# Kernel optimization log

Measured on AMD Instinct MI355X. Metric: run time of the kernel, lower is better.

Reference implementation:

```python
import jax, jax.numpy as jnp
import numpy as np

N = 50000
E = 1600000
D_IN = 512
EPS = 1e-5


def setup_inputs() -> dict:
    key = jax.random.key(0)
    ks = jax.random.split(key, 20)
    p = lambda k, shape: jax.random.normal(k, shape, dtype=jnp.float32) * 0.05
    return {
        "x": jax.random.normal(ks[0], (N, D_IN), dtype=jnp.float32),
        "edge_index": jax.random.randint(ks[1], (2, E), 0, N),
        "edge_weight": jax.random.uniform(ks[2], (E,), dtype=jnp.float32),
        # conv1: ChebConv(512->400) with K=1,2,3 (weight per Chebyshev order)
        "W1a": p(ks[3], (1, D_IN, 400)), "b1a": p(ks[4], (400,)),
        "W1b": p(ks[5], (2, D_IN, 400)), "b1b": p(ks[6], (400,)),
        "W1c": p(ks[7], (3, D_IN, 400)), "b1c": p(ks[8], (400,)),
        "g1": jnp.ones((1200,), jnp.float32), "beta1": jnp.zeros((1200,), jnp.float32),
        # conv2: ChebConv(1200->100) with K=1,2,3
        "W2a": p(ks[9], (1, 1200, 100)), "b2a": p(ks[10], (100,)),
        "W2b": p(ks[11], (2, 1200, 100)), "b2b": p(ks[12], (100,)),
        "W2c": p(ks[13], (3, 1200, 100)), "b2c": p(ks[14], (100,)),
        "g2": jnp.ones((300,), jnp.float32), "beta2": jnp.zeros((300,), jnp.float32),
        "Wl": p(ks[15], (300, 10)), "bl": p(ks[16], (10,)),
    }


def _cheb(x, row, col, norm, W, b):
    """PyG ChebConv forward: out = sum_k T_k(L_hat) x @ W[k] + b.
    L_hat (sym norm, lambda_max=2) = -D^{-1/2} A D^{-1/2}, zero diagonal,
    applied as scatter: (L_hat h)[col] += norm_e * h[row]."""
    K = W.shape[0]
    n = x.shape[0]
    prop = lambda h: jax.ops.segment_sum(norm[:, None] * h[row], col, num_segments=n)
    out = x @ W[0]
    Tx_prev, Tx = x, None
    if K >= 2:
        Tx = prop(x)
        out = out + Tx @ W[1]
    for k in range(2, K):
        Tx_new = 2.0 * prop(Tx) - Tx_prev
        out = out + Tx_new @ W[k]
        Tx_prev, Tx = Tx, Tx_new
    return out + b


def _bn(h, g, beta):
    # BatchNorm over nodes (training-mode batch statistics, biased var)
    mu = h.mean(axis=0)
    var = h.var(axis=0)
    return (h - mu) * jax.lax.rsqrt(var + EPS) * g + beta


def reference(x, edge_index, edge_weight, W1a, b1a, W1b, b1b, W1c, b1c, g1, beta1,
              W2a, b2a, W2b, b2b, W2c, b2c, g2, beta2, Wl, bl):
    row, col = edge_index[0], edge_index[1]
    deg = jax.ops.segment_sum(edge_weight, row, num_segments=x.shape[0])
    safe = jnp.where(deg > 0, deg, 1.0)
    dis = jnp.where(deg > 0, jax.lax.rsqrt(safe), 0.0)  # deg^{-1/2}, inf -> 0
    norm = -dis[row] * edge_weight * dis[col]  # scaled-Laplacian edge weights

    h = jnp.concatenate([
        _cheb(x, row, col, norm, W1a, b1a),
        _cheb(x, row, col, norm, W1b, b1b),
        _cheb(x, row, col, norm, W1c, b1c)], axis=1)  # [N, 1200]
    h = jax.nn.relu(_bn(h, g1, beta1))

    h = jnp.concatenate([
        _cheb(h, row, col, norm, W2a, b2a),
        _cheb(h, row, col, norm, W2b, b2b),
        _cheb(h, row, col, norm, W2c, b2c)], axis=1)  # [N, 300]
    h = _bn(h, g2, beta2)

    logits = h @ Wl + bl  # [N, 10]
    return jax.nn.log_softmax(logits, axis=1)
```

## Files before the change

kernel.cpp:

```cpp
#include <hip/hip_runtime.h>
#include <math.h>

#define EPSB 1e-5f

typedef __attribute__((ext_vector_type(8))) short short8;
typedef __attribute__((ext_vector_type(4))) float floatx4;

__device__ inline float bf2f(unsigned short h) {
  union { unsigned int u; float f; } v; v.u = ((unsigned int)h) << 16; return v.f;
}
__device__ inline unsigned short f2bf(float f) {
  union { float f; unsigned int u; } v; v.f = f;
  unsigned int r = v.u + 0x7fffu + ((v.u >> 16) & 1u);
  return (unsigned short)(r >> 16);
}

__device__ __forceinline__ void gl2lds16(const unsigned short* g, unsigned short* l) {
  __builtin_amdgcn_global_load_lds(
      (const __attribute__((address_space(1))) unsigned int*)g,
      (__attribute__((address_space(3))) unsigned int*)l, 16, 0, 0);
}


__global__ void deg_kernel(const int* __restrict__ row, const float* __restrict__ ew,
                           float* __restrict__ deg, int E) {
  int e = blockIdx.x * blockDim.x + threadIdx.x;
  if (e < E) atomicAdd(&deg[row[e]], ew[e]);
}

__global__ void dis_kernel(float* deg, int n) {
  int i = blockIdx.x * blockDim.x + threadIdx.x;
  if (i < n) { float d = deg[i]; deg[i] = d > 0.f ? rsqrtf(d) : 0.f; }
}

__global__ void count_kernel(const int* __restrict__ col, int* __restrict__ cnt, int E) {
  int e = blockIdx.x * blockDim.x + threadIdx.x;
  if (e < E) atomicAdd(&cnt[col[e]], 1);
}

__global__ __launch_bounds__(1024) void scan_kernel(const int* __restrict__ cnt,
                                                    int* __restrict__ off, int n) {
  __shared__ int buf[1024];
  __shared__ int carry;
  int tid = threadIdx.x;
  if (tid == 0) carry = 0;
  __syncthreads();
  for (int base = 0; base < n; base += 1024) {
    int idx = base + tid;
    int v = (idx < n) ? cnt[idx] : 0;
    buf[tid] = v;
    __syncthreads();
    for (int s = 1; s < 1024; s <<= 1) {
      int t = (tid >= s) ? buf[tid - s] : 0;
      __syncthreads();
      if (tid >= s) buf[tid] += t;
      __syncthreads();
    }
    int total = buf[1023];
    if (idx < n) off[idx] = carry + buf[tid] - v;
    __syncthreads();
    if (tid == 0) carry += total;
    __syncthreads();
  }
  if (tid == 0) off[n] = carry;
}

__global__ void copy_kernel(const int* __restrict__ src, int* __restrict__ dst, int n) {
  int i = blockIdx.x * blockDim.x + threadIdx.x;
  if (i < n) dst[i] = src[i];
}

__global__ void fill_kernel(const int* __restrict__ row, const int* __restrict__ col,
                            const float* __restrict__ ew, const float* __restrict__ dis,
                            int* __restrict__ wptr,
                            int2* __restrict__ ePack, int E) {
  int e = blockIdx.x * blockDim.x + threadIdx.x;
  if (e < E) {
    int r = row[e], c = col[e];
    int p = atomicAdd(&wptr[c], 1);
    float nv = -dis[r] * ew[e] * dis[c];
    ePack[p] = make_int2(r, __float_as_int(nv));
  }
}


__global__ void cast_x_kernel(const float* __restrict__ x, unsigned short* __restrict__ xb,
                              int N) {
  int idx = blockIdx.x * blockDim.x + threadIdx.x;
  if (idx >= N * 128) return;
  int row = idx >> 7, c4 = idx & 127;
  float4 v = *reinterpret_cast<const float4*>(x + (size_t)row * 512 + c4 * 4);
  union { unsigned int u[2]; } p;
  p.u[0] = (unsigned int)f2bf(v.x) | ((unsigned int)f2bf(v.y) << 16);
  p.u[1] = (unsigned int)f2bf(v.z) | ((unsigned int)f2bf(v.w) << 16);
  *reinterpret_cast<uint2*>(xb + (size_t)row * 1536 + c4 * 4) = make_uint2(p.u[0], p.u[1]);
}

__global__ void wprep_kernel(const float* __restrict__ W, unsigned short* __restrict__ Bt,
                             int Ktot, int Nout, int ldBt, int rowOff) {
  int idx = blockIdx.x * blockDim.x + threadIdx.x;
  if (idx >= Ktot * Nout) return;
  int k = idx / Nout, n = idx - k * Nout;
  Bt[(size_t)(rowOff + n) * ldBt + k] = f2bf(W[idx]);
}

__global__ void padzero_kernel(unsigned short* __restrict__ h, int N) {
  int i = blockIdx.x * blockDim.x + threadIdx.x;
  if (i >= N * 2) return;
  *reinterpret_cast<uint4*>(h + (size_t)(i >> 1) * 1216 + 1200 + (i & 1) * 8) =
      make_uint4(0, 0, 0, 0);
}

__global__ void bcat_kernel(const float* __restrict__ a, const float* __restrict__ b,
                            const float* __restrict__ c, float* __restrict__ dst) {
  int i = threadIdx.x;
  if (i < 100) dst[i] = a[i];
  else if (i < 200) dst[i] = b[i - 100];
  else if (i < 300) dst[i] = c[i - 200];
}

__device__ inline void acc8(float* a, uint4 g, float w) {
  a[0] += w * bf2f((unsigned short)(g.x & 0xffff));
  a[1] += w * bf2f((unsigned short)(g.x >> 16));
  a[2] += w * bf2f((unsigned short)(g.y & 0xffff));
  a[3] += w * bf2f((unsigned short)(g.y >> 16));
  a[4] += w * bf2f((unsigned short)(g.z & 0xffff));
  a[5] += w * bf2f((unsigned short)(g.z >> 16));
  a[6] += w * bf2f((unsigned short)(g.w & 0xffff));
  a[7] += w * bf2f((unsigned short)(g.w >> 16));
}

__global__ __launch_bounds__(256) void prop_chunk_kernel(
    unsigned short* __restrict__ base, int ld,
    int srcCol, int dstCol, int subCol,
    const int* __restrict__ off, const int2* __restrict__ ePack,
    float scale, int N) {
  int chunk = blockIdx.x & 7;
  int g = blockIdx.x >> 3;
  int tid = threadIdx.x;
  int slot = (tid >> 3) & 3;
  int c8 = tid & 7;
  int v = g * 8 + (tid >> 5);
  bool valid = v < N;
  int vv = valid ? v : N - 1;
  int co = chunk * 64 + c8 * 8;
  const unsigned short* src = base + srcCol + co;
  int s = off[vv], e = off[vv + 1];
  float a[8] = {}, b[8] = {};
  int i = s + slot;
  for (; i + 12 < e; i += 16) {
    int2 p0 = ePack[i];
    int2 p1 = ePack[i + 4];
    int2 p2 = ePack[i + 8];
    int2 p3 = ePack[i + 12];
    uint4 g0 = *reinterpret_cast<const uint4*>(src + (size_t)p0.x * ld);
    uint4 g1 = *reinterpret_cast<const uint4*>(src + (size_t)p1.x * ld);
    uint4 g2 = *reinterpret_cast<const uint4*>(src + (size_t)p2.x * ld);
    uint4 g3 = *reinterpret_cast<const uint4*>(src + (size_t)p3.x * ld);
    acc8(a, g0, __int_as_float(p0.y));
    acc8(b, g1, __int_as_float(p1.y));
    acc8(a, g2, __int_as_float(p2.y));
    acc8(b, g3, __int_as_float(p3.y));
  }
  for (; i < e; i += 4) {
    int2 p = ePack[i];
    uint4 gg = *reinterpret_cast<const uint4*>(src + (size_t)p.x * ld);
    acc8(a, gg, __int_as_float(p.y));
  }
#pragma unroll
  for (int j = 0; j < 8; j++) a[j] += b[j];
#pragma unroll
  for (int j = 0; j < 8; j++) {
    a[j] += __shfl_xor(a[j], 8);
    a[j] += __shfl_xor(a[j], 16);
  }
  if (slot != 0 || !valid) return;
  if (subCol >= 0) {
    uint4 sv = *reinterpret_cast<const uint4*>(base + subCol + co + (size_t)v * ld);
    a[0] = scale * a[0] - bf2f((unsigned short)(sv.x & 0xffff));
    a[1] = scale * a[1] - bf2f((unsigned short)(sv.x >> 16));
    a[2] = scale * a[2] - bf2f((unsigned short)(sv.y & 0xffff));
    a[3] = scale * a[3] - bf2f((unsigned short)(sv.y >> 16));
    a[4] = scale * a[4] - bf2f((unsigned short)(sv.z & 0xffff));
    a[5] = scale * a[5] - bf2f((unsigned short)(sv.z >> 16));
    a[6] = scale * a[6] - bf2f((unsigned short)(sv.w & 0xffff));
    a[7] = scale * a[7] - bf2f((unsigned short)(sv.w >> 16));
  }
  uint4 o;
  o.x = (unsigned int)f2bf(a[0]) | ((unsigned int)f2bf(a[1]) << 16);
  o.y = (unsigned int)f2bf(a[2]) | ((unsigned int)f2bf(a[3]) << 16);
  o.z = (unsigned int)f2bf(a[4]) | ((unsigned int)f2bf(a[5]) << 16);
  o.w = (unsigned int)f2bf(a[6]) | ((unsigned int)f2bf(a[7]) << 16);
  *reinterpret_cast<uint4*>(base + dstCol + co + (size_t)v * ld) = o;
}

__global__ void prop_z_kernel(const unsigned short* __restrict__ Zcat,
                              const int* __restrict__ off, const int2* __restrict__ ePack,
                              float* __restrict__ h2f, unsigned short* __restrict__ U1) {
  int v = blockIdx.x;
  int f8 = threadIdx.x;
  if (f8 >= 38) return;
  int s = off[v], e = off[v + 1];
  float a[8] = {}, b[8] = {};
  int i = s;
  for (; i + 3 < e; i += 4) {
    int2 p0 = ePack[i];
    int2 p1 = ePack[i + 1];
    int2 p2 = ePack[i + 2];
    int2 p3 = ePack[i + 3];
    uint4 g0 = *reinterpret_cast<const uint4*>(Zcat + (size_t)p0.x * 304 + f8 * 8);
    uint4 g1 = *reinterpret_cast<const uint4*>(Zcat + (size_t)p1.x * 304 + f8 * 8);
    uint4 g2 = *reinterpret_cast<const uint4*>(Zcat + (size_t)p2.x * 304 + f8 * 8);
    uint4 g3 = *reinterpret_cast<const uint4*>(Zcat + (size_t)p3.x * 304 + f8 * 8);
    acc8(a, g0, __int_as_float(p0.y));
    acc8(b, g1, __int_as_float(p1.y));
    acc8(a, g2, __int_as_float(p2.y));
    acc8(b, g3, __int_as_float(p3.y));
  }
  for (; i < e; i++) {
    int2 p = ePack[i];
    uint4 raw = *reinterpret_cast<const uint4*>(Zcat + (size_t)p.x * 304 + f8 * 8);
    acc8(a, raw, __int_as_float(p.y));
  }
#pragma unroll
  for (int j = 0; j < 8; j++) a[j] += b[j];
  if (f8 < 25) {
    float* p = h2f + (size_t)v * 300 + 100 + f8 * 8;
#pragma unroll
    for (int j = 0; j < 8; j++) p[j] += a[j];
  } else {
    uint4 o;
    o.x = (unsigned int)f2bf(a[0]) | ((unsigned int)f2bf(a[1]) << 16);
    o.y = (unsigned int)f2bf(a[2]) | ((unsigned int)f2bf(a[3]) << 16);
    o.z = (unsigned int)f2bf(a[4]) | ((unsigned int)f2bf(a[5]) << 16);
    o.w = (unsigned int)f2bf(a[6]) | ((unsigned int)f2bf(a[7]) << 16);
    *reinterpret_cast<uint4*>(U1 + (size_t)v * 104 + (f8 - 25) * 8) = o;
  }
}

__global__ void prop_u_kernel(const unsigned short* __restrict__ U1,
                              const int* __restrict__ off, const int2* __restrict__ ePack,
                              const unsigned short* __restrict__ Zcat,
                              float* __restrict__ h2f) {
  int v = blockIdx.x;
  int f8 = threadIdx.x;
  if (f8 >= 13) return;
  int s = off[v], e = off[v + 1];
  float a[8] = {}, b[8] = {};
  int i = s;
  for (; i + 3 < e; i += 4) {
    int2 p0 = ePack[i];
    int2 p1 = ePack[i + 1];
    int2 p2 = ePack[i + 2];
    int2 p3 = ePack[i + 3];
    uint4 g0 = *reinterpret_cast<const uint4*>(U1 + (size_t)p0.x * 104 + f8 * 8);
    uint4 g1 = *reinterpret_cast<const uint4*>(U1 + (size_t)p1.x * 104 + f8 * 8);
    uint4 g2 = *reinterpret_cast<const uint4*>(U1 + (size_t)p2.x * 104 + f8 * 8);
    uint4 g3 = *reinterpret_cast<const uint4*>(U1 + (size_t)p3.x * 104 + f8 * 8);
    acc8(a, g0, __int_as_float(p0.y));
    acc8(b, g1, __int_as_float(p1.y));
    acc8(a, g2, __int_as_float(p2.y));
    acc8(b, g3, __int_as_float(p3.y));
  }
  for (; i < e; i++) {
    int2 p = ePack[i];
    uint4 raw = *reinterpret_cast<const uint4*>(U1 + (size_t)p.x * 104 + f8 * 8);
    acc8(a, raw, __int_as_float(p.y));
  }
#pragma unroll
  for (int j = 0; j < 8; j++) a[j] += b[j];
  const unsigned short* z2 = Zcat + (size_t)v * 304 + 200;
  float* p = h2f + (size_t)v * 300 + 200;
#pragma unroll
  for (int j = 0; j < 8; j++) {
    int c = f8 * 8 + j;
    if (c < 100) p[c] += 2.f * a[j] - bf2f(z2[c]);
  }
}

__global__ __launch_bounds__(256) void gemm_bf16_kernel(
    const unsigned short* __restrict__ A, int lda,
    const unsigned short* __restrict__ Bt, int ldb,
    int M, int Nc, int K,
    const float* __restrict__ bias,
    unsigned short* __restrict__ Cb, float* __restrict__ Cf, int ldc, int c0,
    int accumulate) {
  __shared__ __align__(16) unsigned short As[128 * 32];
  __shared__ __align__(16) unsigned short Bs[128 * 32];
  int tid = threadIdx.x;
  int wave = tid >> 6, lane = tid & 63;
  int q = lane >> 4, mn = lane & 15;
  int wr = wave >> 1, wc = wave & 1;
  int row0 = blockIdx.y * 128, col0 = blockIdx.x * 128;
  floatx4 acc[4][4] = {};

  const unsigned short* ga[2];
  const unsigned short* gb[2];
  unsigned short* la[2];
  unsigned short* lb[2];
#pragma unroll
  for (int j = 0; j < 2; j++) {
    int c = j * 256 + tid;
    int r = c >> 2, cw = (c & 3) * 8;
    int gr = row0 + r; if (gr > M - 1) gr = M - 1;
    ga[j] = A + (size_t)gr * lda + cw;
    int gn = col0 + r; if (gn > Nc - 1) gn = Nc - 1;
    gb[j] = Bt + (size_t)gn * ldb + cw;
    la[j] = &As[(j * 256 + wave * 64) * 8];
    lb[j] = &Bs[(j * 256 + wave * 64) * 8];
  }

  for (int k0 = 0; k0 < K; k0 += 32) {
#pragma unroll
    for (int j = 0; j < 2; j++) {
      gl2lds16(ga[j] + k0, la[j]);
      gl2lds16(gb[j] + k0, lb[j]);
    }
    __syncthreads();

    short8 af[4], bf[4];
#pragma unroll
    for (int i = 0; i < 4; i++) {
      af[i] = *reinterpret_cast<const short8*>(&As[(wr * 64 + i * 16 + mn) * 32 + q * 8]);
      bf[i] = *reinterpret_cast<const short8*>(&Bs[(wc * 64 + i * 16 + mn) * 32 + q * 8]);
    }
#pragma unroll
    for (int mi = 0; mi < 4; mi++)
#pragma unroll
      for (int ni = 0; ni < 4; ni++)
        acc[mi][ni] = __builtin_amdgcn_mfma_f32_16x16x32_bf16(af[mi], bf[ni], acc[mi][ni], 0, 0, 0);
    __syncthreads();
  }

#pragma unroll
  for (int mi = 0; mi < 4; mi++) {
#pragma unroll
    for (int ni = 0; ni < 4; ni++) {
      int gcol = col0 + wc * 64 + ni * 16 + mn;
      if (gcol >= Nc) continue;
      float b = bias ? bias[gcol] : 0.f;
#pragma unroll
      for (int r = 0; r < 4; r++) {
        int grow = row0 + wr * 64 + mi * 16 + q * 4 + r;
        if (grow >= M) continue;
        float v = acc[mi][ni][r] + b;
        if (Cb) {
          Cb[(size_t)grow * ldc + c0 + gcol] = f2bf(v);
        } else {
          float* p = Cf + (size_t)grow * ldc + c0 + gcol;
          if (accumulate) v += *p;
          *p = v;
        }
      }
    }
  }
}

__global__ void bn_stats_bf16_kernel(const unsigned short* __restrict__ h, int ld, int C,
                                     int N, float* __restrict__ sums) {
  int c = blockIdx.x * blockDim.x + threadIdx.x;
  if (c >= C) return;
  int r0 = blockIdx.y * 256;
  int r1 = min(N, r0 + 256);
  float s = 0.f, s2 = 0.f;
  for (int r = r0; r < r1; r++) {
    float v = bf2f(h[(size_t)r * ld + c]);
    s += v; s2 += v * v;
  }
  atomicAdd(&sums[c], s);
  atomicAdd(&sums[C + c], s2);
}

__global__ void scsh_kernel(const float* __restrict__ sums, const float* __restrict__ g,
                            const float* __restrict__ beta, float invN, int C,
                            float* __restrict__ scSh) {
  int c = blockIdx.x * blockDim.x + threadIdx.x;
  if (c >= C) return;
  float mu = sums[c] * invN;
  float var = sums[C + c] * invN - mu * mu;
  float s = rsqrtf(var + EPSB) * g[c];
  scSh[c] = s;
  scSh[C + c] = beta[c] - mu * s;
}

__global__ void bn_apply_bf16_kernel(unsigned short* __restrict__ h, int ld, int C8, int N,
                                     const float* __restrict__ scSh, int Cfull, int relu) {
  int idx = blockIdx.x * blockDim.x + threadIdx.x;
  if (idx >= N * C8) return;
  int row = idx / C8, c8 = idx - row * C8;
  unsigned short* p = h + (size_t)row * ld + c8 * 8;
  uint4 raw = *reinterpret_cast<uint4*>(p);
  float v[8];
  v[0] = bf2f((unsigned short)(raw.x & 0xffff)); v[1] = bf2f((unsigned short)(raw.x >> 16));
  v[2] = bf2f((unsigned short)(raw.y & 0xffff)); v[3] = bf2f((unsigned short)(raw.y >> 16));
  v[4] = bf2f((unsigned short)(raw.z & 0xffff)); v[5] = bf2f((unsigned short)(raw.z >> 16));
  v[6] = bf2f((unsigned short)(raw.w & 0xffff)); v[7] = bf2f((unsigned short)(raw.w >> 16));
#pragma unroll
  for (int j = 0; j < 8; j++) {
    int c = c8 * 8 + j;
    float o = v[j] * scSh[c] + scSh[Cfull + c];
    if (relu) o = fmaxf(o, 0.f);
    v[j] = o;
  }
  uint4 o;
  o.x = (unsigned int)f2bf(v[0]) | ((unsigned int)f2bf(v[1]) << 16);
  o.y = (unsigned int)f2bf(v[2]) | ((unsigned int)f2bf(v[3]) << 16);
  o.z = (unsigned int)f2bf(v[4]) | ((unsigned int)f2bf(v[5]) << 16);
  o.w = (unsigned int)f2bf(v[6]) | ((unsigned int)f2bf(v[7]) << 16);
  *reinterpret_cast<uint4*>(p) = o;
}

__global__ void bn_stats_kernel(const float* __restrict__ h, int C, int N,
                                float* __restrict__ sums) {
  int c = blockIdx.x * blockDim.x + threadIdx.x;
  if (c >= C) return;
  int r0 = blockIdx.y * 256;
  int r1 = min(N, r0 + 256);
  float s = 0.f, s2 = 0.f;
  for (int r = r0; r < r1; r++) {
    float v = h[(size_t)r * C + c];
    s += v; s2 += v * v;
  }
  atomicAdd(&sums[c], s);
  atomicAdd(&sums[C + c], s2);
}

__global__ void bn_apply_kernel(float* __restrict__ h, int C, int N,
                                const float* __restrict__ sums, const float* __restrict__ g,
                                const float* __restrict__ beta, float invN, int relu) {
  int C4 = C >> 2;
  int c4 = blockIdx.x * blockDim.x + threadIdx.x;
  if (c4 >= C4) return;
  float sc[4], sh[4];
#pragma unroll
  for (int j = 0; j < 4; j++) {
    int c = c4 * 4 + j;
    float mu = sums[c] * invN;
    float var = sums[C + c] * invN - mu * mu;
    float s = rsqrtf(var + EPSB) * g[c];
    sc[j] = s; sh[j] = beta[c] - mu * s;
  }
  int r0 = blockIdx.y * 256, r1 = min(N, r0 + 256);
  for (int r = r0; r < r1; r++) {
    float4* p = reinterpret_cast<float4*>(h + (size_t)r * C) + c4;
    float4 v = *p;
    v.x = v.x * sc[0] + sh[0]; v.y = v.y * sc[1] + sh[1];
    v.z = v.z * sc[2] + sh[2]; v.w = v.w * sc[3] + sh[3];
    if (relu) {
      v.x = fmaxf(v.x, 0.f); v.y = fmaxf(v.y, 0.f);
      v.z = fmaxf(v.z, 0.f); v.w = fmaxf(v.w, 0.f);
    }
    *p = v;
  }
}


__global__ __launch_bounds__(256) void final_bn_kernel(const float* __restrict__ h2,
                                                       const float* __restrict__ scSh,
                                                       const float* __restrict__ Wl,
                                                       const float* __restrict__ bl,
                                                       float* __restrict__ out, int N) {
  __shared__ float Ws[3000];
  __shared__ float S[600];
  for (int i = threadIdx.x; i < 3000; i += 256) Ws[i] = Wl[i];
  for (int i = threadIdx.x; i < 600; i += 256) S[i] = scSh[i];
  __syncthreads();
  int r = blockIdx.x * blockDim.x + threadIdx.x;
  if (r >= N) return;
  float acc[10];
#pragma unroll
  for (int c = 0; c < 10; c++) acc[c] = bl[c];
  const float* hr = h2 + (size_t)r * 300;
  for (int k = 0; k < 300; k++) {
    float x = hr[k] * S[k] + S[300 + k];
#pragma unroll
    for (int c = 0; c < 10; c++) acc[c] += x * Ws[k * 10 + c];
  }
  float mx = acc[0];
#pragma unroll
  for (int c = 1; c < 10; c++) mx = fmaxf(mx, acc[c]);
  float se = 0.f;
#pragma unroll
  for (int c = 0; c < 10; c++) se += expf(acc[c] - mx);
  float lz = mx + logf(se);
#pragma unroll
  for (int c = 0; c < 10; c++) out[(size_t)r * 10 + c] = acc[c] - lz;
}

__global__ __launch_bounds__(256) void final_kernel(const float* __restrict__ h2,
                                                    const float* __restrict__ Wl,
                                                    const float* __restrict__ bl,
                                                    float* __restrict__ out, int N) {
  __shared__ float Ws[3000];
  for (int i = threadIdx.x; i < 3000; i += 256) Ws[i] = Wl[i];
  __syncthreads();
  int r = blockIdx.x * blockDim.x + threadIdx.x;
  if (r >= N) return;
  float acc[10];
#pragma unroll
  for (int c = 0; c < 10; c++) acc[c] = bl[c];
  const float* hr = h2 + (size_t)r * 300;
  for (int k = 0; k < 300; k++) {
    float x = hr[k];
#pragma unroll
    for (int c = 0; c < 10; c++) acc[c] += x * Ws[k * 10 + c];
  }
  float mx = acc[0];
#pragma unroll
  for (int c = 1; c < 10; c++) mx = fmaxf(mx, acc[c]);
  float se = 0.f;
#pragma unroll
  for (int c = 0; c < 10; c++) se += expf(acc[c] - mx);
  float lz = mx + logf(se);
#pragma unroll
  for (int c = 0; c < 10; c++) out[(size_t)r * 10 + c] = acc[c] - lz;
}


__global__ void prop_kernel(const float* __restrict__ src, int srcLd4, int D4,
                            const int* __restrict__ off, const int2* __restrict__ ePack,
                            float* __restrict__ dst, int dstLd4,
                            const float* __restrict__ sub, int subLd4, float scale) {
  int v = blockIdx.x;
  int f4 = threadIdx.x;
  if (f4 >= D4) return;
  int s = off[v], e = off[v + 1];
  float ax = 0.f, ay = 0.f, az = 0.f, aw = 0.f;
  for (int i = s; i < e; i++) {
    int2 p = ePack[i];
    float w = __int_as_float(p.y);
    const float4 hv = *reinterpret_cast<const float4*>(src + ((size_t)p.x * srcLd4 + f4) * 4);
    ax += w * hv.x; ay += w * hv.y; az += w * hv.z; aw += w * hv.w;
  }
  float4 o;
  if (sub) {
    const float4 sv = *reinterpret_cast<const float4*>(sub + ((size_t)v * subLd4 + f4) * 4);
    o.x = scale * ax - sv.x; o.y = scale * ay - sv.y;
    o.z = scale * az - sv.z; o.w = scale * aw - sv.w;
  } else {
    o.x = ax; o.y = ay; o.z = az; o.w = aw;
  }
  *reinterpret_cast<float4*>(dst + ((size_t)v * dstLd4 + f4) * 4) = o;
}

#define BM 64
#define BN 64
#define BK 16

__global__ __launch_bounds__(256) void gemm_kernel(
    const float* __restrict__ A, int lda,
    const float* __restrict__ B, int ldb,
    float* __restrict__ C, int ldc, int c0,
    int M, int Nc, int K,
    const float* __restrict__ bias, int accumulate) {
  __shared__ float As[BK][BM + 4];
  __shared__ float Bs[BK][BN + 4];
  int tid = threadIdx.x;
  int tx = tid & 15, ty = tid >> 4;
  int row0 = blockIdx.y * BM, col0 = blockIdx.x * BN;
  float acc[4][4] = {};
  int aM = tid >> 2;
  int aK = (tid & 3) << 2;
  int bK = tid >> 4;
  int bN = (tid & 15) << 2;
  for (int k0 = 0; k0 < K; k0 += BK) {
    float4 av = make_float4(0.f, 0.f, 0.f, 0.f);
    int ar = row0 + aM;
    if (ar < M && k0 + aK < K)
      av = *reinterpret_cast<const float4*>(A + (size_t)ar * lda + k0 + aK);
    As[aK + 0][aM] = av.x; As[aK + 1][aM] = av.y;
    As[aK + 2][aM] = av.z; As[aK + 3][aM] = av.w;
    float4 bv = make_float4(0.f, 0.f, 0.f, 0.f);
    int bc = col0 + bN;
    if (bc < Nc && k0 + bK < K)
      bv = *reinterpret_cast<const float4*>(B + (size_t)(k0 + bK) * ldb + bc);
    Bs[bK][bN + 0] = bv.x; Bs[bK][bN + 1] = bv.y;
    Bs[bK][bN + 2] = bv.z; Bs[bK][bN + 3] = bv.w;
    __syncthreads();
#pragma unroll
    for (int k = 0; k < BK; k++) {
      float a0 = As[k][ty * 4 + 0], a1 = As[k][ty * 4 + 1];
      float a2 = As[k][ty * 4 + 2], a3 = As[k][ty * 4 + 3];
      float b0 = Bs[k][tx * 4 + 0], b1 = Bs[k][tx * 4 + 1];
      float b2 = Bs[k][tx * 4 + 2], b3 = Bs[k][tx * 4 + 3];
      acc[0][0] += a0 * b0; acc[0][1] += a0 * b1; acc[0][2] += a0 * b2; acc[0][3] += a0 * b3;
      acc[1][0] += a1 * b0; acc[1][1] += a1 * b1; acc[1][2] += a1 * b2; acc[1][3] += a1 * b3;
      acc[2][0] += a2 * b0; acc[2][1] += a2 * b1; acc[2][2] += a2 * b2; acc[2][3] += a2 * b3;
      acc[3][0] += a3 * b0; acc[3][1] += a3 * b1; acc[3][2] += a3 * b2; acc[3][3] += a3 * b3;
    }
    __syncthreads();
  }
#pragma unroll
  for (int i = 0; i < 4; i++) {
    int r = row0 + ty * 4 + i;
    if (r >= M) continue;
#pragma unroll
    for (int j = 0; j < 4; j++) {
      int c = col0 + tx * 4 + j;
      if (c >= Nc) continue;
      float v = acc[i][j];
      if (bias) v += bias[c];
      float* p = C + (size_t)r * ldc + c0 + c;
      if (accumulate) *p += v; else *p = v;
    }
  }
}


extern "C" void kernel_launch(void* const* d_in, const int* in_sizes, int n_in,
                              void* d_out, int out_size, void* d_ws, size_t ws_size,
                              hipStream_t stream) {
  const float* x   = (const float*)d_in[0];
  const int*   ei  = (const int*)d_in[1];
  const float* ew  = (const float*)d_in[2];
  const float* W1a = (const float*)d_in[3];
  const float* b1a = (const float*)d_in[4];
  const float* W1b = (const float*)d_in[5];
  const float* b1b = (const float*)d_in[6];
  const float* W1c = (const float*)d_in[7];
  const float* b1c = (const float*)d_in[8];
  const float* g1  = (const float*)d_in[9];
  const float* be1 = (const float*)d_in[10];
  const float* W2a = (const float*)d_in[11];
  const float* b2a = (const float*)d_in[12];
  const float* W2b = (const float*)d_in[13];
  const float* b2b = (const float*)d_in[14];
  const float* W2c = (const float*)d_in[15];
  const float* b2c = (const float*)d_in[16];
  const float* g2  = (const float*)d_in[17];
  const float* be2 = (const float*)d_in[18];
  const float* Wl  = (const float*)d_in[19];
  const float* bl  = (const float*)d_in[20];
  float* out = (float*)d_out;

  const int N = in_sizes[0] / 512;
  const int E = in_sizes[1] / 2;
  const int* row = ei;
  const int* col = ei + E;
  (void)n_in; (void)out_size;

  int eb = (E + 255) / 256;
  int nb = (N + 255) / 256;

  char* ws = (char*)d_ws;
  size_t o = 0;
  int2*  ePack = (int2*)(ws + o);  o += (size_t)E * 8;
  float* dis   = (float*)(ws + o); o += (size_t)N * 4;
  int*   cnt   = (int*)(ws + o);   o += (size_t)N * 4;
  int*   off   = (int*)(ws + o);   o += (size_t)(N + 4) * 4;
  int*   wptr  = (int*)(ws + o);   o += (size_t)N * 4;
  float* sums  = (float*)(ws + o); o += 2400 * 4;
  float* scSh  = (float*)(ws + o); o += 2400 * 4;
  float* bcat  = (float*)(ws + o); o += 304 * 4;
  o = (o + 255) & ~(size_t)255;
  size_t oCommon = o;

  size_t oA = oCommon;
  unsigned short* Bt1a = (unsigned short*)(ws + oA); oA += (size_t)400 * 512 * 2;
  unsigned short* Bt1b = (unsigned short*)(ws + oA); oA += (size_t)400 * 1024 * 2;
  unsigned short* Bt1c = (unsigned short*)(ws + oA); oA += (size_t)400 * 1536 * 2;
  unsigned short* Bt2cat0 = (unsigned short*)(ws + oA); oA += (size_t)304 * 1216 * 2;
  unsigned short* Bt2z    = (unsigned short*)(ws + oA); oA += (size_t)304 * 1216 * 2;
  oA = (oA + 255) & ~(size_t)255;
  unsigned short* h1n = (unsigned short*)(ws + oA); oA += (size_t)N * 1216 * 2;
  oA = (oA + 255) & ~(size_t)255;
  float* h2f = (float*)(ws + oA); oA += (size_t)N * 300 * 4;
  oA = (oA + 255) & ~(size_t)255;
  unsigned short* Xcat = (unsigned short*)(ws + oA); oA += (size_t)N * 1536 * 2;
  unsigned short* Zcat = Xcat;
  unsigned short* U1 = Xcat + (size_t)N * 304;

  bool planA = (ws_size >= oA);

  hipMemsetAsync(dis, 0, (size_t)N * 4, stream);
  hipMemsetAsync(cnt, 0, (size_t)N * 4, stream);
  deg_kernel<<<eb, 256, 0, stream>>>(row, ew, dis, E);
  dis_kernel<<<nb, 256, 0, stream>>>(dis, N);
  count_kernel<<<eb, 256, 0, stream>>>(col, cnt, E);
  scan_kernel<<<1, 1024, 0, stream>>>(cnt, off, N);
  copy_kernel<<<nb, 256, 0, stream>>>(off, wptr, N);
  fill_kernel<<<eb, 256, 0, stream>>>(row, col, ew, dis, wptr, ePack, E);

  if (planA) {
    wprep_kernel<<<(400 * 512 + 255) / 256, 256, 0, stream>>>(W1a, Bt1a, 512, 400, 512, 0);
    wprep_kernel<<<(400 * 1024 + 255) / 256, 256, 0, stream>>>(W1b, Bt1b, 1024, 400, 1024, 0);
    wprep_kernel<<<(400 * 1536 + 255) / 256, 256, 0, stream>>>(W1c, Bt1c, 1536, 400, 1536, 0);
    hipMemsetAsync(Bt2cat0, 0, (size_t)304 * 1216 * 2, stream);
    hipMemsetAsync(Bt2z, 0, (size_t)304 * 1216 * 2, stream);
    wprep_kernel<<<(100 * 1200 + 255) / 256, 256, 0, stream>>>(W2a, Bt2cat0, 1200, 100, 1216, 0);
    wprep_kernel<<<(100 * 1200 + 255) / 256, 256, 0, stream>>>(W2b, Bt2cat0, 1200, 100, 1216, 100);
    wprep_kernel<<<(100 * 1200 + 255) / 256, 256, 0, stream>>>(W2c, Bt2cat0, 1200, 100, 1216, 200);
    wprep_kernel<<<(100 * 1200 + 255) / 256, 256, 0, stream>>>(W2b + 1200 * 100, Bt2z, 1200, 100, 1216, 0);
    wprep_kernel<<<(100 * 1200 + 255) / 256, 256, 0, stream>>>(W2c + 1200 * 100, Bt2z, 1200, 100, 1216, 100);
    wprep_kernel<<<(100 * 1200 + 255) / 256, 256, 0, stream>>>(W2c + 2 * 1200 * 100, Bt2z, 1200, 100, 1216, 200);
    bcat_kernel<<<1, 320, 0, stream>>>(b2a, b2b, b2c, bcat);
    cast_x_kernel<<<(N * 128 + 255) / 256, 256, 0, stream>>>(x, Xcat, N);
    padzero_kernel<<<(N * 2 + 255) / 256, 256, 0, stream>>>(h1n, N);

    int gridP = ((N + 7) / 8) * 8;
    prop_chunk_kernel<<<gridP, 256, 0, stream>>>(Xcat, 1536, 0, 512, -1,
                                                 off, ePack, 1.f, N);
    prop_chunk_kernel<<<gridP, 256, 0, stream>>>(Xcat, 1536, 512, 1024, 0,
                                                 off, ePack, 2.f, N);

    dim3 gA((400 + 127) / 128, (N + 127) / 128);
    gemm_bf16_kernel<<<gA, 256, 0, stream>>>(Xcat, 1536, Bt1a, 512, N, 400, 512,
                                             b1a, h1n, nullptr, 1216, 0, 0);
    gemm_bf16_kernel<<<gA, 256, 0, stream>>>(Xcat, 1536, Bt1b, 1024, N, 400, 1024,
                                             b1b, h1n, nullptr, 1216, 400, 0);
    gemm_bf16_kernel<<<gA, 256, 0, stream>>>(Xcat, 1536, Bt1c, 1536, N, 400, 1536,
                                             b1c, h1n, nullptr, 1216, 800, 0);

    hipMemsetAsync(sums, 0, 2400 * 4, stream);
    dim3 s1g((1200 + 255) / 256, (N + 255) / 256);
    bn_stats_bf16_kernel<<<s1g, 256, 0, stream>>>(h1n, 1216, 1200, N, sums);
    scsh_kernel<<<(1200 + 255) / 256, 256, 0, stream>>>(sums, g1, be1, 1.f / (float)N, 1200, scSh);
    bn_apply_bf16_kernel<<<((size_t)N * 150 + 255) / 256, 256, 0, stream>>>(
        h1n, 1216, 150, N, scSh, 1200, 1);

    dim3 gB0((300 + 127) / 128, (N + 127) / 128);
    gemm_bf16_kernel<<<gB0, 256, 0, stream>>>(h1n, 1216, Bt2cat0, 1216, N, 300, 1216,
                                              bcat, nullptr, h2f, 300, 0, 0);

    dim3 gBz((304 + 127) / 128, (N + 127) / 128);
    gemm_bf16_kernel<<<gBz, 256, 0, stream>>>(h1n, 1216, Bt2z, 1216, N, 304, 1216,
                                              nullptr, Zcat, nullptr, 304, 0, 0);

    prop_z_kernel<<<N, 64, 0, stream>>>(Zcat, off, ePack, h2f, U1);
    prop_u_kernel<<<N, 64, 0, stream>>>(U1, off, ePack, Zcat, h2f);

    hipMemsetAsync(sums, 0, 2400 * 4, stream);
    dim3 s2g((300 + 255) / 256, (N + 255) / 256);
    bn_stats_kernel<<<s2g, 256, 0, stream>>>(h2f, 300, N, sums);
    scsh_kernel<<<(300 + 255) / 256, 256, 0, stream>>>(sums, g2, be2, 1.f / (float)N, 300, scSh);
    final_bn_kernel<<<nb, 256, 0, stream>>>(h2f, scSh, Wl, bl, out, N);
    return;
  }

  size_t oB = oCommon;
  float* h2 = (float*)(ws + oB); oB += (size_t)N * 300 * 4;
  oB = (oB + 255) & ~(size_t)255;
  float* h1 = (float*)(ws + oB); oB += (size_t)N * 1200 * 4;
  oB = (oB + 255) & ~(size_t)255;
  size_t avail = (ws_size > oB) ? (ws_size - oB) : 0;
  int C1 = 64;
  { const int opts[4] = {512, 256, 128, 64};
    for (int i = 0; i < 4; i++)
      if ((size_t)2 * N * opts[i] * 4 <= avail) { C1 = opts[i]; break; } }
  int C2 = 100;
  { const int opts[6] = {1200, 600, 400, 300, 200, 100};
    for (int i = 0; i < 6; i++)
      if ((size_t)2 * N * opts[i] * 4 <= avail) { C2 = opts[i]; break; } }
  int maxC = C1 > C2 ? C1 : C2;
  float* S1 = (float*)(ws + oB);
  float* S2 = S1 + (size_t)N * maxC;

  dim3 g1d((400 + BN - 1) / BN, (N + BM - 1) / BM);
  gemm_kernel<<<g1d, 256, 0, stream>>>(x, 512, W1a, 400, h1, 1200, 0,   N, 400, 512, b1a, 0);
  gemm_kernel<<<g1d, 256, 0, stream>>>(x, 512, W1b, 400, h1, 1200, 400, N, 400, 512, b1b, 0);
  gemm_kernel<<<g1d, 256, 0, stream>>>(x, 512, W1c, 400, h1, 1200, 800, N, 400, 512, b1c, 0);
  for (int c = 0; c < 512; c += C1) {
    int D4 = C1 / 4;
    int bt = ((D4 + 63) / 64) * 64;
    prop_kernel<<<N, bt, 0, stream>>>(x + c, 128, D4, off, ePack, S1, D4, nullptr, 0, 1.f);
    gemm_kernel<<<g1d, 256, 0, stream>>>(S1, C1, W1b + (size_t)(512 + c) * 400, 400, h1, 1200, 400, N, 400, C1, nullptr, 1);
    gemm_kernel<<<g1d, 256, 0, stream>>>(S1, C1, W1c + (size_t)(512 + c) * 400, 400, h1, 1200, 800, N, 400, C1, nullptr, 1);
    prop_kernel<<<N, bt, 0, stream>>>(S1, D4, D4, off, ePack, S2, D4, x + c, 128, 2.f);
    gemm_kernel<<<g1d, 256, 0, stream>>>(S2, C1, W1c + (size_t)(2 * 512 + c) * 400, 400, h1, 1200, 800, N, 400, C1, nullptr, 1);
  }

  hipMemsetAsync(sums, 0, 2400 * 4, stream);
  dim3 s1g((1200 + 255) / 256, (N + 255) / 256);
  bn_stats_kernel<<<s1g, 256, 0, stream>>>(h1, 1200, N, sums);
  dim3 a1g((300 + 63) / 64, (N + 255) / 256);
  bn_apply_kernel<<<a1g, 64, 0, stream>>>(h1, 1200, N, sums, g1, be1, 1.f / (float)N, 1);

  dim3 g2d((100 + BN - 1) / BN, (N + BM - 1) / BM);
  gemm_kernel<<<g2d, 256, 0, stream>>>(h1, 1200, W2a, 100, h2, 300, 0,   N, 100, 1200, b2a, 0);
  gemm_kernel<<<g2d, 256, 0, stream>>>(h1, 1200, W2b, 100, h2, 300, 100, N, 100, 1200, b2b, 0);
  gemm_kernel<<<g2d, 256, 0, stream>>>(h1, 1200, W2c, 100, h2, 300, 200, N, 100, 1200, b2c, 0);
  for (int c = 0; c < 1200; c += C2) {
    int D4 = C2 / 4;
    int bt = ((D4 + 63) / 64) * 64;
    prop_kernel<<<N, bt, 0, stream>>>(h1 + c, 300, D4, off, ePack, S1, D4, nullptr, 0, 1.f);
    gemm_kernel<<<g2d, 256, 0, stream>>>(S1, C2, W2b + (size_t)(1200 + c) * 100, 100, h2, 300, 100, N, 100, C2, nullptr, 1);
    gemm_kernel<<<g2d, 256, 0, stream>>>(S1, C2, W2c + (size_t)(1200 + c) * 100, 100, h2, 300, 200, N, 100, C2, nullptr, 1);
    prop_kernel<<<N, bt, 0, stream>>>(S1, D4, D4, off, ePack, S2, D4, h1 + c, 300, 2.f);
    gemm_kernel<<<g2d, 256, 0, stream>>>(S2, C2, W2c + (size_t)(2 * 1200 + c) * 100, 100, h2, 300, 200, N, 100, C2, nullptr, 1);
  }

  hipMemsetAsync(sums, 0, 2400 * 4, stream);
  dim3 s2g((300 + 255) / 256, (N + 255) / 256);
  bn_stats_kernel<<<s2g, 256, 0, stream>>>(h2, 300, N, sums);
  dim3 a2g((75 + 63) / 64, (N + 255) / 256);
  bn_apply_kernel<<<a2g, 64, 0, stream>>>(h2, 300, N, sums, g2, be2, 1.f / (float)N, 0);

  final_kernel<<<nb, 256, 0, stream>>>(h2, Wl, bl, out, N);
}
```

Before: 1.938 ms.

## Parallelize CSR scan, fuse degree/count atomics, use packed FMA in gathers

Replaces the single-block serial scan with a three-pass multi-block scan and merges the degree and count atomic kernels into one launch. In the propagation kernels, per-element bf16 FMAs become v_pk_fma_f32 via inline asm. In prop_chunk, each of the four slots now takes a contiguous quarter of a node's edge range instead of interleaving every fourth edge. These target preprocessing latency and ALU pressure in the gathers, at the cost of extra launches and less compiler visibility through inline asm.

```diff
diff --git a/kernel.cpp b/kernel.cpp
--- a/kernel.cpp
+++ b/kernel.cpp
@@ -5,6 +5,7 @@
 
 typedef __attribute__((ext_vector_type(8))) short short8;
 typedef __attribute__((ext_vector_type(4))) float floatx4;
+typedef __attribute__((ext_vector_type(2))) float floatx2;
 
 __device__ inline float bf2f(unsigned short h) {
   union { unsigned int u; float f; } v; v.u = ((unsigned int)h) << 16; return v.f;
@@ -21,11 +22,27 @@
       (__attribute__((address_space(3))) unsigned int*)l, 16, 0, 0);
 }
 
-
-__global__ void deg_kernel(const int* __restrict__ row, const float* __restrict__ ew,
-                           float* __restrict__ deg, int E) {
+__device__ __forceinline__ void pk4(floatx2* a, uint4 g, floatx2 wv) {
+  unsigned int u[4] = {g.x, g.y, g.z, g.w};
+#pragma unroll
+  for (int j = 0; j < 4; j++) {
+    union { unsigned int q; float f; } lo, hi;
+    lo.q = u[j] << 16;
+    hi.q = u[j] & 0xffff0000u;
+    floatx2 v; v[0] = lo.f; v[1] = hi.f;
+    asm("v_pk_fma_f32 %0, %1, %2, %0" : "+v"(a[j]) : "v"(v), "v"(wv));
+  }
+}
+
+
+__global__ void degcnt_kernel(const int* __restrict__ row, const int* __restrict__ col,
+                              const float* __restrict__ ew,
+                              float* __restrict__ deg, int* __restrict__ cnt, int E) {
   int e = blockIdx.x * blockDim.x + threadIdx.x;
-  if (e < E) atomicAdd(&deg[row[e]], ew[e]);
+  if (e < E) {
+    atomicAdd(&deg[row[e]], ew[e]);
+    atomicAdd(&cnt[col[e]], 1);
+  }
 }
 
 __global__ void dis_kernel(float* deg, int n) {
@@ -33,36 +50,37 @@
   if (i < n) { float d = deg[i]; deg[i] = d > 0.f ? rsqrtf(d) : 0.f; }
 }
 
-__global__ void count_kernel(const int* __restrict__ col, int* __restrict__ cnt, int E) {
-  int e = blockIdx.x * blockDim.x + threadIdx.x;
-  if (e < E) atomicAdd(&cnt[col[e]], 1);
-}
-
-__global__ __launch_bounds__(1024) void scan_kernel(const int* __restrict__ cnt,
-                                                    int* __restrict__ off, int n) {
+__global__ __launch_bounds__(1024) void scan1_kernel(const int* __restrict__ cnt,
+                                                     int* __restrict__ off,
+                                                     int* __restrict__ bsum, int n) {
   __shared__ int buf[1024];
-  __shared__ int carry;
   int tid = threadIdx.x;
-  if (tid == 0) carry = 0;
+  int idx = blockIdx.x * 1024 + tid;
+  int v = (idx < n) ? cnt[idx] : 0;
+  buf[tid] = v;
   __syncthreads();
-  for (int base = 0; base < n; base += 1024) {
-    int idx = base + tid;
-    int v = (idx < n) ? cnt[idx] : 0;
-    buf[tid] = v;
+  for (int s = 1; s < 1024; s <<= 1) {
+    int t = (tid >= s) ? buf[tid - s] : 0;
     __syncthreads();
-    for (int s = 1; s < 1024; s <<= 1) {
-      int t = (tid >= s) ? buf[tid - s] : 0;
-      __syncthreads();
-      if (tid >= s) buf[tid] += t;
-      __syncthreads();
-    }
-    int total = buf[1023];
-    if (idx < n) off[idx] = carry + buf[tid] - v;
+    if (tid >= s) buf[tid] += t;
     __syncthreads();
-    if (tid == 0) carry += total;
-    __syncthreads();
-  }
-  if (tid == 0) off[n] = carry;
+  }
+  if (idx < n) off[idx] = buf[tid] - v;
+  if (tid == 1023) bsum[blockIdx.x] = buf[1023];
+}
+
+__global__ void scan2_kernel(int* __restrict__ bsum, int* __restrict__ off,
+                             int nb, int n) {
+  if (threadIdx.x == 0 && blockIdx.x == 0) {
+    int run = 0;
+    for (int k = 0; k < nb; k++) { int t = bsum[k]; bsum[k] = run; run += t; }
+    off[n] = run;
+  }
+}
+
+__global__ void scan3_kernel(int* __restrict__ off, const int* __restrict__ bsum, int n) {
+  int i = blockIdx.x * blockDim.x + threadIdx.x;
+  if (i < n) off[i] += bsum[i >> 10];
 }
 
 __global__ void copy_kernel(const int* __restrict__ src, int* __restrict__ dst, int n) {
@@ -117,17 +135,6 @@
   if (i < 100) dst[i] = a[i];
   else if (i < 200) dst[i] = b[i - 100];
   else if (i < 300) dst[i] = c[i - 200];
-}
-
-__device__ inline void acc8(float* a, uint4 g, float w) {
-  a[0] += w * bf2f((unsigned short)(g.x & 0xffff));
-  a[1] += w * bf2f((unsigned short)(g.x >> 16));
-  a[2] += w * bf2f((unsigned short)(g.y & 0xffff));
-  a[3] += w * bf2f((unsigned short)(g.y >> 16));
-  a[4] += w * bf2f((unsigned short)(g.z & 0xffff));
-  a[5] += w * bf2f((unsigned short)(g.z >> 16));
-  a[6] += w * bf2f((unsigned short)(g.w & 0xffff));
-  a[7] += w * bf2f((unsigned short)(g.w >> 16));
 }
 
 __global__ __launch_bounds__(256) void prop_chunk_kernel(
@@ -146,29 +153,41 @@
   int co = chunk * 64 + c8 * 8;
   const unsigned short* src = base + srcCol + co;
   int s = off[vv], e = off[vv + 1];
-  float a[8] = {}, b[8] = {};
-  int i = s + slot;
-  for (; i + 12 < e; i += 16) {
+  int len = e - s;
+  int s0 = s + (len * slot >> 2);
+  int e0 = s + (len * (slot + 1) >> 2);
+  floatx2 a2[4] = {}, b2[4] = {};
+  int i = s0;
+  for (; i + 3 < e0; i += 4) {
     int2 p0 = ePack[i];
-    int2 p1 = ePack[i + 4];
-    int2 p2 = ePack[i + 8];
-    int2 p3 = ePack[i + 12];
+    int2 p1 = ePack[i + 1];
+    int2 p2 = ePack[i + 2];
+    int2 p3 = ePack[i + 3];
     uint4 g0 = *reinterpret_cast<const uint4*>(src + (size_t)p0.x * ld);
     uint4 g1 = *reinterpret_cast<const uint4*>(src + (size_t)p1.x * ld);
     uint4 g2 = *reinterpret_cast<const uint4*>(src + (size_t)p2.x * ld);
     uint4 g3 = *reinterpret_cast<const uint4*>(src + (size_t)p3.x * ld);
-    acc8(a, g0, __int_as_float(p0.y));
-    acc8(b, g1, __int_as_float(p1.y));
-    acc8(a, g2, __int_as_float(p2.y));
-    acc8(b, g3, __int_as_float(p3.y));
-  }
-  for (; i < e; i += 4) {
+    floatx2 w0; w0[0] = w0[1] = __int_as_float(p0.y);
+    floatx2 w1; w1[0] = w1[1] = __int_as_float(p1.y);
+    floatx2 w2; w2[0] = w2[1] = __int_as_float(p2.y);
+    floatx2 w3; w3[0] = w3[1] = __int_as_float(p3.y);
+    pk4(a2, g0, w0);
+    pk4(b2, g1, w1);
+    pk4(a2, g2, w2);
+    pk4(b2, g3, w3);
+  }
+  for (; i < e0; i++) {
     int2 p = ePack[i];
     uint4 gg = *reinterpret_cast<const uint4*>(src + (size_t)p.x * ld);
-    acc8(a, gg, __int_as_float(p.y));
-  }
-#pragma unroll
-  for (int j = 0; j < 8; j++) a[j] += b[j];
+    floatx2 wv; wv[0] = wv[1] = __int_as_float(p.y);
+    pk4(a2, gg, wv);
+  }
+  float a[8];
+#pragma unroll
+  for (int j = 0; j < 4; j++) {
+    a[2 * j]     = a2[j][0] + b2[j][0];
+    a[2 * j + 1] = a2[j][1] + b2[j][1];
+  }
 #pragma unroll
   for (int j = 0; j < 8; j++) {
     a[j] += __shfl_xor(a[j], 8);
@@ -201,7 +220,7 @@
   int f8 = threadIdx.x;
   if (f8 >= 38) return;
   int s = off[v], e = off[v + 1];
-  float a[8] = {}, b[8] = {};
+  floatx2 a2[4] = {}, b2[4] = {};
   int i = s;
   for (; i + 3 < e; i += 4) {
     int2 p0 = ePack[i];
@@ -212,18 +231,27 @@
     uint4 g1 = *reinterpret_cast<const uint4*>(Zcat + (size_t)p1.x * 304 + f8 * 8);
     uint4 g2 = *reinterpret_cast<const uint4*>(Zcat + (size_t)p2.x * 304 + f8 * 8);
     uint4 g3 = *reinterpret_cast<const uint4*>(Zcat + (size_t)p3.x * 304 + f8 * 8);
-    acc8(a, g0, __int_as_float(p0.y));
-    acc8(b, g1, __int_as_float(p1.y));
-    acc8(a, g2, __int_as_float(p2.y));
-    acc8(b, g3, __int_as_float(p3.y));
+    floatx2 w0; w0[0] = w0[1] = __int_as_float(p0.y);
+    floatx2 w1; w1[0] = w1[1] = __int_as_float(p1.y);
+    floatx2 w2; w2[0] = w2[1] = __int_as_float(p2.y);
+    floatx2 w3; w3[0] = w3[1] = __int_as_float(p3.y);
+    pk4(a2, g0, w0);
+    pk4(b2, g1, w1);
+    pk4(a2, g2, w2);
+    pk4(b2, g3, w3);
   }
   for (; i < e; i++) {
     int2 p = ePack[i];
     uint4 raw = *reinterpret_cast<const uint4*>(Zcat + (size_t)p.x * 304 + f8 * 8);
-    acc8(a, raw, __int_as_float(p.y));
-  }
-#pragma unroll
-  for (int j = 0; j < 8; j++) a[j] += b[j];
+    floatx2 wv; wv[0] = wv[1] = __int_as_float(p.y);
+    pk4(a2, raw, wv);
+  }
+  float a[8];
+#pragma unroll
+  for (int j = 0; j < 4; j++) {
+    a[2 * j]     = a2[j][0] + b2[j][0];
+    a[2 * j + 1] = a2[j][1] + b2[j][1];
+  }
   if (f8 < 25) {
     float* p = h2f + (size_t)v * 300 + 100 + f8 * 8;
 #pragma unroll
@@ -246,7 +274,7 @@
   int f8 = threadIdx.x;
   if (f8 >= 13) return;
   int s = off[v], e = off[v + 1];
-  float a[8] = {}, b[8] = {};
+  floatx2 a2[4] = {}, b2[4] = {};
   int i = s;
   for (; i + 3 < e; i += 4) {
     int2 p0 = ePack[i];
@@ -257,18 +285,27 @@
     uint4 g1 = *reinterpret_cast<const uint4*>(U1 + (size_t)p1.x * 104 + f8 * 8);
     uint4 g2 = *reinterpret_cast<const uint4*>(U1 + (size_t)p2.x * 104 + f8 * 8);
     uint4 g3 = *reinterpret_cast<const uint4*>(U1 + (size_t)p3.x * 104 + f8 * 8);
-    acc8(a, g0, __int_as_float(p0.y));
-    acc8(b, g1, __int_as_float(p1.y));
-    acc8(a, g2, __int_as_float(p2.y));
-    acc8(b, g3, __int_as_float(p3.y));
+    floatx2 w0; w0[0] = w0[1] = __int_as_float(p0.y);
+    floatx2 w1; w1[0] = w1[1] = __int_as_float(p1.y);
+    floatx2 w2; w2[0] = w2[1] = __int_as_float(p2.y);
+    floatx2 w3; w3[0] = w3[1] = __int_as_float(p3.y);
+    pk4(a2, g0, w0);
+    pk4(b2, g1, w1);
+    pk4(a2, g2, w2);
+    pk4(b2, g3, w3);
   }
   for (; i < e; i++) {
     int2 p = ePack[i];
     uint4 raw = *reinterpret_cast<const uint4*>(U1 + (size_t)p.x * 104 + f8 * 8);
-    acc8(a, raw, __int_as_float(p.y));
-  }
-#pragma unroll
-  for (int j = 0; j < 8; j++) a[j] += b[j];
+    floatx2 wv; wv[0] = wv[1] = __int_as_float(p.y);
+    pk4(a2, raw, wv);
+  }
+  float a[8];
+#pragma unroll
+  for (int j = 0; j < 4; j++) {
+    a[2 * j]     = a2[j][0] + b2[j][0];
+    a[2 * j + 1] = a2[j][1] + b2[j][1];
+  }
   const unsigned short* z2 = Zcat + (size_t)v * 304 + 200;
   float* p = h2f + (size_t)v * 300 + 200;
 #pragma unroll
@@ -641,6 +678,7 @@
 
   int eb = (E + 255) / 256;
   int nb = (N + 255) / 256;
+  int nb1 = (N + 1023) / 1024;
 
   char* ws = (char*)d_ws;
   size_t o = 0;
@@ -649,6 +687,7 @@
   int*   cnt   = (int*)(ws + o);   o += (size_t)N * 4;
   int*   off   = (int*)(ws + o);   o += (size_t)(N + 4) * 4;
   int*   wptr  = (int*)(ws + o);   o += (size_t)N * 4;
+  int*   bsum  = (int*)(ws + o);   o += (size_t)(nb1 + 4) * 4;
   float* sums  = (float*)(ws + o); o += 2400 * 4;
   float* scSh  = (float*)(ws + o); o += 2400 * 4;
   float* bcat  = (float*)(ws + o); o += 304 * 4;
@@ -674,10 +713,11 @@
 
   hipMemsetAsync(dis, 0, (size_t)N * 4, stream);
   hipMemsetAsync(cnt, 0, (size_t)N * 4, stream);
-  deg_kernel<<<eb, 256, 0, stream>>>(row, ew, dis, E);
+  degcnt_kernel<<<eb, 256, 0, stream>>>(row, col, ew, dis, cnt, E);
   dis_kernel<<<nb, 256, 0, stream>>>(dis, N);
-  count_kernel<<<eb, 256, 0, stream>>>(col, cnt, E);
-  scan_kernel<<<1, 1024, 0, stream>>>(cnt, off, N);
+  scan1_kernel<<<nb1, 1024, 0, stream>>>(cnt, off, bsum, N);
+  scan2_kernel<<<1, 64, 0, stream>>>(bsum, off, nb1, N);
+  scan3_kernel<<<nb, 256, 0, stream>>>(off, bsum, N);
   copy_kernel<<<nb, 256, 0, stream>>>(off, wptr, N);
   fill_kernel<<<eb, 256, 0, stream>>>(row, col, ew, dis, wptr, ePack, E);
 
```

New measurement: 1.853 ms. 4.4% less time.
